# Performance work log

Hardware: AMD Instinct MI355X
Metric: run time of the kernel (lower is better)

Reference implementation:

```python
import jax, jax.numpy as jnp
import numpy as np

SR = 22050
HOP = 512
BINS_PER_OCTAVE = 24
N_OCTAVES = 7
N_BINS = BINS_PER_OCTAVE * N_OCTAVES  # 168
FMIN = 32.7  # center_bins with bins_per_semitone=1 leaves fmin unchanged


def _make_cqt_kernels():
    """Right-aligned (causal) complex CQT kernels, 24 bins/octave, 7 octaves.

    This is the explicit math the stateful SlidingCqt24 C++ routine computes
    incrementally: for each bin k with center freq f_k = fmin * 2^(k/24),
    a Hann-windowed complex exponential of length N_k = ceil(Q*sr/f_k),
    Q = 1/(2^(1/24)-1). Bins are ordered ascending in frequency, matching the
    per-octave np.flip layout of the original forward.
    """
    Q = 1.0 / (2.0 ** (1.0 / BINS_PER_OCTAVE) - 1.0)
    freqs = FMIN * 2.0 ** (np.arange(N_BINS) / BINS_PER_OCTAVE)
    lens = np.ceil(Q * SR / freqs).astype(np.int64)
    n_max = int(lens.max())  # 23014
    kr = np.zeros((N_BINS, n_max), dtype=np.float32)
    ki = np.zeros((N_BINS, n_max), dtype=np.float32)
    for k in range(N_BINS):  # small fixed loop over 168 bins (setup only)
        n = int(lens[k])
        t = np.arange(n)
        win = np.hanning(n)
        c = win * np.exp(2j * np.pi * freqs[k] * t / SR) / n
        kr[k, n_max - n:] = c.real.astype(np.float32)
        ki[k, n_max - n:] = c.imag.astype(np.float32)
    return kr, ki


def setup_inputs() -> dict:
    key = jax.random.key(0)
    audio = jax.random.normal(key, (4, 1, 352768), dtype=jnp.float32)
    kr, ki = _make_cqt_kernels()
    return {
        "audio_waveforms": audio,
        "kern_real": jnp.asarray(kr),
        "kern_imag": jnp.asarray(ki),
    }


def reference(audio_waveforms, kern_real, kern_imag):
    # audio: [B, C, S]; kernels: [K, Nmax]
    n_max = kern_real.shape[1]
    B, C, S = audio_waveforms.shape
    n_blocks = S // HOP  # 689
    # Causal sliding window: block i analyzes the n_max samples ending at
    # sample (i+1)*HOP (left zero-pad for early blocks), matching the
    # block-streaming behavior of the sliding CQT.
    pad = n_max - HOP
    x = jnp.pad(audio_waveforms, ((0, 0), (0, 0), (pad, 0)))
    # Strided frame gather: [n_blocks, Nmax] index table.
    idx = jnp.arange(n_blocks)[:, None] * HOP + jnp.arange(n_max)[None, :]
    frames = x[..., idx]  # [B, C, T, Nmax]
    re = jnp.einsum("bctn,kn->bctk", frames, kern_real)
    im = jnp.einsum("bctn,kn->bctk", frames, kern_imag)
    mag = jnp.sqrt(re * re + im * im)  # [B, C, n_blocks, n_bins]
    return mag
```

## Files before the change

### kernel.cpp

```cpp
#include <hip/hip_runtime.h>
#include <math.h>


namespace {
constexpr int kSR    = 22050;
constexpr int kHop   = 512;
constexpr int kBins  = 168;
constexpr int kT     = 689;
constexpr int kB     = 4;
constexpr int kS     = 352768;
constexpr float kKScale    = 4096.0f;
constexpr float kKScaleInv = 1.0f / 4096.0f;
constexpr int kG16 = 11;
constexpr int kFBB = 44;
constexpr int kAcc = kB * kT * kBins * 2;
constexpr int kTPadB   = 768;
constexpr int kBinPadB = 176;
constexpr int kAccB    = kB * kTPadB * kBinPadB * 2;
}

typedef _Float16 half8 __attribute__((ext_vector_type(8)));
typedef _Float16 half2v __attribute__((ext_vector_type(2)));
typedef float floatx4 __attribute__((ext_vector_type(4)));

struct Jobs {
  int k0[48];
  int lo[48];
  int hi[48];
  int n;
};

struct JobsC {
  int lo16[kG16];
  int cb16[kG16];
  int mlo[3];
  int sm[24];
  int slo[24];
  int shi[24];
  int sbeg[3];
  int scnt[3];
  int ns;
  int totch;
};

__device__ inline void atomAddF(float* p, float v) {
  __hip_atomic_fetch_add(p, v, __ATOMIC_RELAXED, __HIP_MEMORY_SCOPE_AGENT);
}

typedef __attribute__((address_space(3))) unsigned int lds_uint;
typedef __attribute__((address_space(1))) const unsigned int glb_uint;
__device__ __forceinline__ void dma16(const void* g, void* l) {
  __builtin_amdgcn_global_load_lds((glb_uint*)g, (lds_uint*)l, 16, 0, 0);
}

__global__ __launch_bounds__(256) void prep_fused(
    const float* __restrict__ x, const float* __restrict__ kr,
    const float* __restrict__ ki, _Float16* __restrict__ xp,
    _Float16* __restrict__ bp, float* __restrict__ accb,
    const int pad, const int xps, const int nmax,
    const int nbx, const int nbp, const JobsC jt) {
  int bid = blockIdx.x;
  const int tid = threadIdx.x;

  if (bid < nbx) {
    const int octx = xps >> 3;
    const int gid = bid * 256 + tid;
    if (gid >= kB * octx) return;
    const int b = gid / octx;
    const int i = (gid - b * octx) * 8;
    const float* xb = x + (size_t)b * kS - pad;
    half8 h;
    #pragma unroll
    for (int j = 0; j < 8; ++j) {
      const int e = i + j;
      h[j] = (e >= pad && e < pad + kS) ? (_Float16)xb[e] : (_Float16)0.f;
    }
    *(half8*)&xp[(size_t)b * xps + i] = h;
    return;
  }
  bid -= nbx;

  if (bid < nbp) {
    const int chunkid = bid * 4 + (tid >> 6);
    const int lane = tid & 63;
    if (chunkid >= jt.totch) return;
    int g = 0;
    #pragma unroll
    for (int j = 1; j < kG16; ++j)
      if (chunkid >= jt.cb16[j]) g = j;
    const int c = chunkid - jt.cb16[g];
    const int mm = lane & 15;
    const int q  = lane >> 4;
    const int bin  = g * 16 + mm;
    const int col0 = jt.lo16[g] + c * 32 + q * 8;
    const bool binok = (bin < kBins);
    const float* rowr = kr + (size_t)bin * nmax;
    const float* rowi = ki + (size_t)bin * nmax;
    half8 hre, him;
    #pragma unroll
    for (int j = 0; j < 8; ++j) {
      const int col = col0 + j;
      const bool ok = binok && (col < nmax);
      hre[j] = ok ? (_Float16)(rowr[col] * kKScale) : (_Float16)0.f;
      him[j] = ok ? (_Float16)(rowi[col] * kKScale) : (_Float16)0.f;
    }
    _Float16* dst = bp + (size_t)chunkid * 1024 + lane * 8;
    *(half8*)dst = hre;
    *(half8*)(dst + 512) = him;
    return;
  }
  bid -= nbp;

  const int idx = (bid * 256 + tid) * 4;
  if (idx < kAcc)
    *(floatx4*)&accb[idx] = (floatx4){0.f, 0.f, 0.f, 0.f};
}

template <bool PARTIAL>
__global__ __launch_bounds__(256) void cqt_mfma_t(
    const _Float16* __restrict__ bp, const _Float16* __restrict__ xp,
    float* __restrict__ accb, _Float16* __restrict__ part,
    const int xps, const JobsC jt) {
  __shared__ _Float16 lds[2][12288];

  const int sx = blockIdx.y;
  const int fb = blockIdx.x >> 2;
  const int b  = blockIdx.x & 3;
  const int tid  = threadIdx.x;
  const int wave = tid >> 6;
  const int lane = tid & 63;
  const int mm = lane & 15;
  const int q  = lane >> 4;
  const int mac = jt.sm[sx];
  const int g16 = mac * 4 + wave;
  const bool gvalid = (g16 < kG16);
  const int mlo = jt.mlo[mac];
  const int gs = gvalid ? ((jt.lo16[g16] - mlo) >> 5) : 0x7fffffff;
  const int slo = jt.slo[sx];
  const int shi = jt.shi[sx];
  const int fbase = fb * 64;

  const _Float16* xb = xp + (size_t)b * xps;
  int aoff0, aoff1;
  {
    const int r0 = wave * 2;
    int row0 = fbase + (r0 & 3) * 16 + mm;
    if (row0 > kT - 1) row0 = kT - 1;
    aoff0 = row0 * kHop + (r0 >> 2) * 32 + q * 8;
    const int r1 = r0 + 1;
    int row1 = fbase + (r1 & 3) * 16 + mm;
    if (row1 > kT - 1) row1 = kT - 1;
    aoff1 = row1 * kHop + (r1 >> 2) * 32 + q * 8;
  }
  const _Float16* bgrp =
      gvalid ? (bp + (size_t)(jt.cb16[g16] - gs) * 1024 + lane * 8) : bp;

  floatx4 accr[4], acci[4];
  #pragma unroll
  for (int tl = 0; tl < 4; ++tl) {
    accr[tl] = (floatx4){0.f, 0.f, 0.f, 0.f};
    acci[tl] = (floatx4){0.f, 0.f, 0.f, 0.f};
  }

  auto stageDMA = [&](int c, int buf) {
    _Float16* L = lds[buf];
    const _Float16* xc = xb + mlo + c * 32;
    dma16(xc + aoff0, L + (wave * 2) * 512);
    dma16(xc + aoff1, L + (wave * 2 + 1) * 512);
    if (gvalid && c >= gs) {
      const _Float16* bs = bgrp + (size_t)c * 1024;
      #pragma unroll
      for (int cc = 0; cc < 2; ++cc)
        #pragma unroll
        for (int ri = 0; ri < 2; ++ri)
          dma16(bs + cc * 1024 + ri * 512,
                L + 4096 + (wave * 4 + cc * 2 + ri) * 512);
    }
  };

  auto compute = [&](int c, int buf) {
    if (!gvalid || c < gs) return;
    const _Float16* L = lds[buf];
    #pragma unroll
    for (int cc = 0; cc < 2; ++cc) {
      const half8 Bre = *(const half8*)(L + 4096 + (wave * 4 + cc * 2) * 512 + lane * 8);
      const half8 Bim = *(const half8*)(L + 4096 + (wave * 4 + cc * 2 + 1) * 512 + lane * 8);
      #pragma unroll
      for (int tl = 0; tl < 4; ++tl) {
        const half8 A = *(const half8*)(L + (cc * 4 + tl) * 512 + lane * 8);
        accr[tl] = __builtin_amdgcn_mfma_f32_16x16x32_f16(A, Bre, accr[tl], 0, 0, 0);
        acci[tl] = __builtin_amdgcn_mfma_f32_16x16x32_f16(A, Bim, acci[tl], 0, 0, 0);
      }
    }
  };

  stageDMA(slo, 0);
  int buf = 0;
  #pragma unroll 1
  for (int c = slo; c < shi; c += 2) {
    __syncthreads();
    if (c + 2 < shi) stageDMA(c + 2, buf ^ 1);
    compute(c, buf);
    buf ^= 1;
  }

  if (PARTIAL) {
    _Float16* pw = part +
        (((size_t)sx * kFBB + blockIdx.x) * 4 + wave) * 2048 + lane * 32;
    #pragma unroll
    for (int tl = 0; tl < 4; ++tl) {
      half8 p;
      #pragma unroll
      for (int r = 0; r < 4; ++r) {
        p[r * 2]     = (_Float16)accr[tl][r];
        p[r * 2 + 1] = (_Float16)acci[tl][r];
      }
      *(half8*)(pw + tl * 8) = p;
    }
  } else {
    const int bin = g16 * 16 + mm;
    if (bin < kBins) {
      #pragma unroll
      for (int tl = 0; tl < 4; ++tl) {
        const int tb = fbase + tl * 16 + q * 4;
        #pragma unroll
        for (int r = 0; r < 4; ++r) {
          const int t = tb + r;
          if (t < kT) {
            const size_t o = (((size_t)b * kT + t) * kBins + bin) * 2;
            atomAddF(&accb[o],     accr[tl][r] * kKScaleInv);
            atomAddF(&accb[o + 1], acci[tl][r] * kKScaleInv);
          }
        }
      }
    }
  }
}

__global__ __launch_bounds__(256) void cqt_mag_part(
    const _Float16* __restrict__ part, float* __restrict__ out,
    const JobsC jt) {
  const int fbb = blockIdx.x;
  const int fb = fbb >> 2;
  const int b  = fbb & 3;
  const int wave = threadIdx.x >> 6;
  const int lane = threadIdx.x & 63;
  const int g16 = blockIdx.y * 4 + wave;
  if (g16 >= kG16) return;
  const int mac = g16 >> 2;
  const int w   = g16 & 3;
  const int mm = lane & 15;
  const int q  = lane >> 4;

  float a[32];
  #pragma unroll
  for (int i = 0; i < 32; ++i) a[i] = 0.f;
  const int s0 = jt.sbeg[mac];
  const int s1 = s0 + jt.scnt[mac];
  #pragma unroll 1
  for (int s = s0; s < s1; ++s) {
    const _Float16* p = part +
        (((size_t)s * kFBB + fbb) * 4 + w) * 2048 + lane * 32;
    #pragma unroll
    for (int tl = 0; tl < 4; ++tl) {
      const half8 v = *(const half8*)(p + tl * 8);
      #pragma unroll
      for (int j = 0; j < 8; ++j) a[tl * 8 + j] += (float)v[j];
    }
  }
  const int k = g16 * 16 + mm;
  if (k >= kBins) return;
  #pragma unroll
  for (int tl = 0; tl < 4; ++tl) {
    #pragma unroll
    for (int r = 0; r < 4; ++r) {
      const int t = fb * 64 + tl * 16 + q * 4 + r;
      if (t < kT) {
        const float re = a[tl * 8 + r * 2];
        const float im = a[tl * 8 + r * 2 + 1];
        out[((size_t)b * kT + t) * kBins + k] =
            sqrtf(re * re + im * im) * kKScaleInv;
      }
    }
  }
}

__global__ __launch_bounds__(256) void cqt_mag4(
    const float* __restrict__ accb, float* __restrict__ out) {
  const int gid = (blockIdx.x * 256 + threadIdx.x) * 4;
  if (gid >= kB * kT * kBins) return;
  const floatx4 v0 = *(const floatx4*)&accb[gid * 2];
  const floatx4 v1 = *(const floatx4*)&accb[gid * 2 + 4];
  floatx4 o;
  o[0] = sqrtf(v0[0] * v0[0] + v0[1] * v0[1]);
  o[1] = sqrtf(v0[2] * v0[2] + v0[3] * v0[3]);
  o[2] = sqrtf(v1[0] * v1[0] + v1[1] * v1[1]);
  o[3] = sqrtf(v1[2] * v1[2] + v1[3] * v1[3]);
  *(floatx4*)&out[gid] = o;
}

__global__ __launch_bounds__(256) void cqt_mag_final(
    const float* __restrict__ accb, float* __restrict__ out,
    const int tp, const int kp) {
  int gid = blockIdx.x * 256 + threadIdx.x;
  if (gid >= kB * kT * kBins) return;
  const int k = gid % kBins;
  const int r = gid / kBins;
  const int t = r % kT;
  const int b = r / kT;
  const float2 v = ((const float2*)accb)[((size_t)b * tp + t) * kp + k];
  out[gid] = sqrtf(v.x * v.x + v.y * v.y);
}

__global__ __launch_bounds__(256) void prep_x_kernel(
    const float* __restrict__ x, _Float16* __restrict__ xp,
    const int pad, const int xps) {
  const int halfx = xps >> 1;
  int gid = blockIdx.x * 256 + threadIdx.x;
  if (gid >= kB * halfx) return;
  const int b = gid / halfx;
  const int i = (gid - b * halfx) * 2;
  float v0 = 0.f, v1 = 0.f;
  if (i     >= pad && i     < pad + kS) v0 = x[(size_t)b * kS + (i - pad)];
  if (i + 1 >= pad && i + 1 < pad + kS) v1 = x[(size_t)b * kS + (i + 1 - pad)];
  half2v h; h.x = (_Float16)v0; h.y = (_Float16)v1;
  *(half2v*)&xp[(size_t)b * xps + i] = h;
}

__global__ __launch_bounds__(256) void cqt_mfma_kernel(
    const float* __restrict__ kr, const float* __restrict__ ki,
    const _Float16* __restrict__ xp, float* __restrict__ accb,
    const int nmax, const int xps, const Jobs jt) {
  __shared__ _Float16 Bs[2][16][264];
  const int jb = blockIdx.x;
  const int k0   = jt.k0[jb];
  const int n_lo = jt.lo[jb];
  const int n_hi = jt.hi[jb];
  const int b  = blockIdx.z;
  const int fb = blockIdx.y;
  const int tid  = threadIdx.x;
  const int lane = tid & 63;
  const int wave = tid >> 6;
  const int m = lane & 15;
  const int q = lane >> 4;
  const int sbin = tid >> 4;
  const int scol = tid & 15;
  const int gbin = k0 + sbin;
  const bool binok = (gbin < kBins);
  const float* rowr = kr + (size_t)gbin * nmax;
  const float* rowi = ki + (size_t)gbin * nmax;
  const int fbase = fb * 256 + wave * 64;
  const _Float16* ax =
      xp + (size_t)b * xps + (size_t)(fbase + m) * kHop + q * 8;
  floatx4 accr[4], acci[4];
  #pragma unroll
  for (int tl = 0; tl < 4; ++tl) {
    accr[tl] = (floatx4){0.f, 0.f, 0.f, 0.f};
    acci[tl] = (floatx4){0.f, 0.f, 0.f, 0.f};
  }
  for (int n0r = n_lo; n0r < n_hi; n0r += 256) {
    __syncthreads();
    #pragma unroll
    for (int c = 0; c < 16; ++c) {
      const int col = n0r + scol + c * 16;
      const bool ok = binok && (col < nmax);
      const float vr = ok ? rowr[col] : 0.f;
      const float vi = ok ? rowi[col] : 0.f;
      Bs[0][sbin][scol + c * 16] = (_Float16)(vr * kKScale);
      Bs[1][sbin][scol + c * 16] = (_Float16)(vi * kKScale);
    }
    __syncthreads();
    const _Float16* axr = ax + n0r;
    #pragma unroll
    for (int c = 0; c < 8; ++c) {
      const int ko = c * 32 + q * 8;
      const half8 br = *(const half8*)&Bs[0][m][ko];
      const half8 bi = *(const half8*)&Bs[1][m][ko];
      #pragma unroll
      for (int tl = 0; tl < 4; ++tl) {
        const half8 a = *(const half8*)(axr + tl * 16 * kHop + c * 32);
        accr[tl] = __builtin_amdgcn_mfma_f32_16x16x32_f16(a, br, accr[tl], 0, 0, 0);
        acci[tl] = __builtin_amdgcn_mfma_f32_16x16x32_f16(a, bi, acci[tl], 0, 0, 0);
      }
    }
  }
  #pragma unroll
  for (int tl = 0; tl < 4; ++tl) {
    #pragma unroll
    for (int rr = 0; rr < 4; ++rr) {
      const int t = fbase + tl * 16 + q * 4 + rr;
      const size_t o = (((size_t)b * kTPadB + t) * kBinPadB + (k0 + m)) * 2;
      atomAddF(&accb[o],     accr[tl][rr] * kKScaleInv);
      atomAddF(&accb[o + 1], acci[tl][rr] * kKScaleInv);
    }
  }
}

namespace fb32 {
constexpr int TT = 8;
constexpr int KG = 4;
constexpr int kTTiles  = (kT + TT - 1) / TT;
constexpr int kKGroups = kBins / KG;
constexpr int kWaves   = kB * kTTiles * kKGroups;
}

__global__ __launch_bounds__(256) void cqt_mag_kernel(
    const float* __restrict__ x,
    const float* __restrict__ kr,
    const float* __restrict__ ki,
    float* __restrict__ out,
    const int nmax, const int pad) {
  using namespace fb32;
  const int wave = (blockIdx.x << 2) + (threadIdx.x >> 6);
  const int lane = threadIdx.x & 63;
  if (wave >= kWaves) return;
  const int kg    = wave / (kB * kTTiles);
  const int rem   = wave - kg * (kB * kTTiles);
  const int b     = rem / kTTiles;
  const int ttile = rem - b * kTTiles;
  const int k0 = kg * KG;
  const int t0 = ttile * TT;
  const double Q  = 1.0 / (exp2(1.0 / 24.0) - 1.0);
  const double f0 = 32.7 * exp2((double)k0 / 24.0);
  int N = (int)ceil(Q * (double)kSR / f0) + 8;
  int full_start = nmax - N;
  if (full_start < 0) full_start = 0;
  int tbase[TT], lo[TT], t_last;
  { int t = t0 + TT - 1; if (t > kT - 1) t = kT - 1; t_last = t; }
  #pragma unroll
  for (int tt = 0; tt < TT; ++tt) {
    int t = t0 + tt; if (t > kT - 1) t = kT - 1;
    tbase[tt] = b * kS + t * kHop - pad;
    lo[tt]    = pad - t * kHop;
  }
  int head_start = pad - t_last * kHop;
  if (head_start < full_start) head_start = full_start;
  int safe = pad - t0 * kHop;
  if (safe < head_start) safe = head_start;
  int body_start = nmax - ((nmax - safe) & ~63);
  float accr[TT][KG], acci[TT][KG];
  #pragma unroll
  for (int tt = 0; tt < TT; ++tt)
    #pragma unroll
    for (int kk = 0; kk < KG; ++kk) { accr[tt][kk] = 0.f; acci[tt][kk] = 0.f; }
  for (int n = body_start - 64; n > head_start - 64; n -= 64) {
    const int nn = n + lane;
    const bool kok = (nn >= 0);
    float krv[KG], kiv[KG];
    #pragma unroll
    for (int kk = 0; kk < KG; ++kk) {
      krv[kk] = kok ? kr[(k0 + kk) * nmax + nn] : 0.f;
      kiv[kk] = kok ? ki[(k0 + kk) * nmax + nn] : 0.f;
    }
    float a[TT];
    #pragma unroll
    for (int tt = 0; tt < TT; ++tt)
      a[tt] = (nn >= lo[tt]) ? x[tbase[tt] + nn] : 0.f;
    #pragma unroll
    for (int tt = 0; tt < TT; ++tt)
      #pragma unroll
      for (int kk = 0; kk < KG; ++kk) {
        accr[tt][kk] = fmaf(a[tt], krv[kk], accr[tt][kk]);
        acci[tt][kk] = fmaf(a[tt], kiv[kk], acci[tt][kk]);
      }
  }
  for (int n = body_start; n < nmax; n += 64) {
    const int nn = n + lane;
    float krv[KG], kiv[KG];
    #pragma unroll
    for (int kk = 0; kk < KG; ++kk) {
      krv[kk] = kr[(k0 + kk) * nmax + nn];
      kiv[kk] = ki[(k0 + kk) * nmax + nn];
    }
    float a[TT];
    #pragma unroll
    for (int tt = 0; tt < TT; ++tt)
      a[tt] = x[tbase[tt] + nn];
    #pragma unroll
    for (int tt = 0; tt < TT; ++tt)
      #pragma unroll
      for (int kk = 0; kk < KG; ++kk) {
        accr[tt][kk] = fmaf(a[tt], krv[kk], accr[tt][kk]);
        acci[tt][kk] = fmaf(a[tt], kiv[kk], acci[tt][kk]);
      }
  }
  #pragma unroll
  for (int tt = 0; tt < TT; ++tt) {
    #pragma unroll
    for (int kk = 0; kk < KG; ++kk) {
      float r = accr[tt][kk];
      float i = acci[tt][kk];
      #pragma unroll
      for (int s = 32; s > 0; s >>= 1) {
        r += __shfl_xor(r, s, 64);
        i += __shfl_xor(i, s, 64);
      }
      if (lane == 0) {
        const int t = t0 + tt;
        if (t < kT)
          out[(b * kT + t) * kBins + (k0 + kk)] = sqrtf(r * r + i * i);
      }
    }
  }
}

extern "C" void kernel_launch(void* const* d_in, const int* in_sizes, int n_in,
                              void* d_out, int out_size, void* d_ws, size_t ws_size,
                              hipStream_t stream) {
  const float* x  = (const float*)d_in[0];
  const float* kr = (const float*)d_in[1];
  const float* ki = (const float*)d_in[2];
  float* out = (float*)d_out;

  const int nmax = in_sizes[1] / kBins;
  const int pad  = nmax - kHop;

  const int kcap = ((nmax + 255) / 256) * 256;
  const double Q = 1.0 / (exp2(1.0 / 24.0) - 1.0);

  JobsC jc;
  int tot = 0;
  for (int g = 0; g < kG16; ++g) {
    const double f0 = 32.7 * exp2((double)(16 * g) / 24.0);
    const int N = (int)ceil(Q * (double)kSR / f0) + 8;
    int lo = nmax - N;
    if (lo < 0) lo = 0;
    lo &= ~255;
    jc.lo16[g] = lo;
    jc.cb16[g] = tot;
    tot += (kcap - lo) / 32;
  }
  jc.totch = tot;
  int ns = 0;
  for (int m = 0; m < 3; ++m) {
    jc.mlo[m] = jc.lo16[4 * m];
    jc.sbeg[m] = ns;
    const int C = (kcap - jc.mlo[m]) / 32;
    const int nsl = (C + 95) / 96;
    const int len = ((C + nsl - 1) / nsl + 1) & ~1;
    for (int s = 0; s < nsl && ns < 24; ++s) {
      const int lo = s * len;
      if (lo >= C) break;
      int hi = lo + len;
      if (hi > C) hi = C;
      jc.sm[ns] = m; jc.slo[ns] = lo; jc.shi[ns] = hi;
      ++ns;
    }
    jc.scnt[m] = ns - jc.sbeg[m];
  }
  jc.ns = ns;

  const int xpsA = (kT - 1) * kHop + kcap + 256;
  const size_t xpA_bytes = (size_t)kB * xpsA * sizeof(_Float16);
  const size_t bpA_bytes = (size_t)tot * 2048;

  const size_t partP_off   = (xpA_bytes + 511) & ~(size_t)511;
  const size_t partP_bytes = (size_t)ns * kFBB * 4 * 2048 * sizeof(_Float16);
  const size_t bpP_off     = (partP_off + partP_bytes + 511) & ~(size_t)511;
  const size_t ws_P = bpP_off + bpA_bytes;

  const size_t accA_off  = (xpA_bytes + 511) & ~(size_t)511;
  const size_t accA_bytes = (size_t)kAcc * sizeof(float);
  const size_t bpA_off   = (accA_off + accA_bytes + 511) & ~(size_t)511;
  const size_t ws_A = bpA_off + bpA_bytes;

  const int xpsB = (kTPadB - 1) * kHop + kcap + 256;
  const size_t xpB_bytes = (size_t)kB * xpsB * sizeof(_Float16);
  const size_t accB_off  = (xpB_bytes + 511) & ~(size_t)511;
  const size_t accB_bytes = (size_t)kAccB * sizeof(float);
  const size_t ws_B = accB_off + accB_bytes;

  const int nbx = (kB * (xpsA / 8) + 255) / 256;
  const int nbp = (tot + 3) / 4;

  if (ws_size >= ws_P) {
    _Float16* xp   = (_Float16*)d_ws;
    _Float16* part = (_Float16*)((char*)d_ws + partP_off);
    _Float16* bp   = (_Float16*)((char*)d_ws + bpP_off);

    prep_fused<<<nbx + nbp, 256, 0, stream>>>(
        x, kr, ki, xp, bp, (float*)part , pad, xpsA, nmax,
        nbx, nbp, jc);
    {
      dim3 grid(kFBB, ns);
      cqt_mfma_t<true><<<grid, 256, 0, stream>>>(
          bp, xp, nullptr, part, xpsA, jc);
    }
    {
      dim3 grid(kFBB, 3);
      cqt_mag_part<<<grid, 256, 0, stream>>>(part, out, jc);
    }
    return;
  }

  if (ws_size >= ws_A) {
    _Float16* xp = (_Float16*)d_ws;
    float* accb  = (float*)((char*)d_ws + accA_off);
    _Float16* bp = (_Float16*)((char*)d_ws + bpA_off);

    const int nba = (kAcc / 4 + 255) / 256;
    prep_fused<<<nbx + nbp + nba, 256, 0, stream>>>(
        x, kr, ki, xp, bp, accb, pad, xpsA, nmax, nbx, nbp, jc);
    {
      dim3 grid(kFBB, ns);
      cqt_mfma_t<false><<<grid, 256, 0, stream>>>(
          bp, xp, accb, nullptr, xpsA, jc);
    }
    {
      const int total = kB * kT * kBins;
      cqt_mag4<<<(total / 4 + 255) / 256, 256, 0, stream>>>(accb, out);
    }
    return;
  }

  if (ws_size >= ws_B) {
    _Float16* xp = (_Float16*)d_ws;
    float* accb  = (float*)((char*)d_ws + accB_off);
    Jobs jt;
    int nj = 0;
    for (int g = 0; g < 11; ++g) {
      const int gk0 = 16 * g;
      const double f0 = 32.7 * exp2((double)gk0 / 24.0);
      const int N = (int)ceil(Q * (double)kSR / f0) + 8;
      int lo = nmax - N;
      if (lo < 0) lo = 0;
      lo = (lo / 2048) * 2048;
      for (int s = lo; s < kcap && nj < 48; s += 2048) {
        jt.k0[nj] = gk0;
        jt.lo[nj] = s;
        jt.hi[nj] = (s + 2048 < kcap) ? s + 2048 : kcap;
        ++nj;
      }
    }
    jt.n = nj;
    hipMemsetAsync(accb, 0, accB_bytes, stream);
    {
      const int total = kB * (xpsB / 2);
      prep_x_kernel<<<(total + 255) / 256, 256, 0, stream>>>(x, xp, pad, xpsB);
    }
    {
      dim3 grid(nj, kTPadB / 256, kB);
      cqt_mfma_kernel<<<grid, 256, 0, stream>>>(kr, ki, xp, accb, nmax, xpsB, jt);
    }
    {
      const int total = kB * kT * kBins;
      cqt_mag_final<<<(total + 255) / 256, 256, 0, stream>>>(
          accb, out, kTPadB, kBinPadB);
    }
    return;
  }

  {
    const int blocks = fb32::kWaves / 4;
    cqt_mag_kernel<<<blocks, 256, 0, stream>>>(x, kr, ki, out, nmax, pad);
  }
}
```

Baseline: 119.8 us.

## Triple-buffer LDS DMA pipeline with uniform loads and XCD-aware block remap

Moves the MFMA CQT kernel from double to triple LDS buffering, so two stages are in flight, using an explicit vmcnt wait and raw barrier in place of __syncthreads. The B-kernel DMA is made unconditional, clamping the chunk index, so every wave issues the same number of loads and the fixed vmcnt count holds. Workgroup indices are also remapped so neighbouring blocks land on the same XCD, for better L2 reuse. This costs 50% more shared memory, which may lower occupancy, plus some redundant B loads for waves that have not started or are invalid.

After: 125.8 us. 5.0% more time.

```diff
diff --git a/kernel.cpp b/kernel.cpp
--- a/kernel.cpp
+++ b/kernel.cpp
@@ -121,11 +121,19 @@
     const _Float16* __restrict__ bp, const _Float16* __restrict__ xp,
     float* __restrict__ accb, _Float16* __restrict__ part,
     const int xps, const JobsC jt) {
-  __shared__ _Float16 lds[2][12288];
-
-  const int sx = blockIdx.y;
-  const int fb = blockIdx.x >> 2;
-  const int b  = blockIdx.x & 3;
+  __shared__ _Float16 lds[3][12288];
+
+  const int nwg = kFBB * gridDim.y;
+  int lin = blockIdx.y * kFBB + blockIdx.x;
+  {
+    const int q = nwg >> 3, r = nwg & 7;
+    const int xcd = lin & 7, idx = lin >> 3;
+    lin = (xcd < r ? xcd * (q + 1) : r * (q + 1) + (xcd - r) * q) + idx;
+  }
+  const int sx  = lin / kFBB;
+  const int fbb = lin - sx * kFBB;
+  const int fb = fbb >> 2;
+  const int b  = fbb & 3;
   const int tid  = threadIdx.x;
   const int wave = tid >> 6;
   const int lane = tid & 63;
@@ -135,7 +143,7 @@
   const int g16 = mac * 4 + wave;
   const bool gvalid = (g16 < kG16);
   const int mlo = jt.mlo[mac];
-  const int gs = gvalid ? ((jt.lo16[g16] - mlo) >> 5) : 0x7fffffff;
+  const int gs = gvalid ? ((jt.lo16[g16] - mlo) >> 5) : 0;
   const int slo = jt.slo[sx];
   const int shi = jt.shi[sx];
   const int fbase = fb * 64;
@@ -153,7 +161,8 @@
     aoff1 = row1 * kHop + (r1 >> 2) * 32 + q * 8;
   }
   const _Float16* bgrp =
-      gvalid ? (bp + (size_t)(jt.cb16[g16] - gs) * 1024 + lane * 8) : bp;
+      gvalid ? (bp + (size_t)(jt.cb16[g16] - gs) * 1024 + lane * 8)
+             : (bp + lane * 8);
 
   floatx4 accr[4], acci[4];
   #pragma unroll
@@ -167,15 +176,14 @@
     const _Float16* xc = xb + mlo + c * 32;
     dma16(xc + aoff0, L + (wave * 2) * 512);
     dma16(xc + aoff1, L + (wave * 2 + 1) * 512);
-    if (gvalid && c >= gs) {
-      const _Float16* bs = bgrp + (size_t)c * 1024;
-      #pragma unroll
-      for (int cc = 0; cc < 2; ++cc)
-        #pragma unroll
-        for (int ri = 0; ri < 2; ++ri)
-          dma16(bs + cc * 1024 + ri * 512,
-                L + 4096 + (wave * 4 + cc * 2 + ri) * 512);
-    }
+    const int cb = gvalid ? (c > gs ? c : gs) : 0;
+    const _Float16* bs = bgrp + (size_t)cb * 1024;
+    #pragma unroll
+    for (int cc = 0; cc < 2; ++cc)
+      #pragma unroll
+      for (int ri = 0; ri < 2; ++ri)
+        dma16(bs + cc * 1024 + ri * 512,
+              L + 4096 + (wave * 4 + cc * 2 + ri) * 512);
   };
 
   auto compute = [&](int c, int buf) {
@@ -194,19 +202,23 @@
     }
   };
 
+  const int cN = shi - 2;
   stageDMA(slo, 0);
-  int buf = 0;
+  stageDMA(slo + 2 <= cN ? slo + 2 : cN, 1);
+  int j = 0;
   #pragma unroll 1
-  for (int c = slo; c < shi; c += 2) {
-    __syncthreads();
-    if (c + 2 < shi) stageDMA(c + 2, buf ^ 1);
-    compute(c, buf);
-    buf ^= 1;
+  for (int c = slo; c < shi; c += 2, ++j) {
+    asm volatile("s_waitcnt vmcnt(6)" ::: "memory");
+    __builtin_amdgcn_s_barrier();
+    __builtin_amdgcn_sched_barrier(0);
+    int cn = c + 4; if (cn > cN) cn = cN;
+    stageDMA(cn, (j + 2) % 3);
+    compute(c, j % 3);
   }
 
   if (PARTIAL) {
     _Float16* pw = part +
-        (((size_t)sx * kFBB + blockIdx.x) * 4 + wave) * 2048 + lane * 32;
+        (((size_t)sx * kFBB + fbb) * 4 + wave) * 2048 + lane * 32;
     #pragma unroll
     for (int tl = 0; tl < 4; ++tl) {
       half8 p;
@@ -219,7 +231,7 @@
     }
   } else {
     const int bin = g16 * 16 + mm;
-    if (bin < kBins) {
+    if (gvalid && bin < kBins) {
       #pragma unroll
       for (int tl = 0; tl < 4; ++tl) {
         const int tb = fbase + tl * 16 + q * 4;
```

## Load B fragments directly to registers and remap workgroups across XCDs

Applied to the files above, without the earlier changes.

Per-wave B (kernel) fragments are now read from global memory straight into registers inside compute, instead of being DMA-staged through LDS. This shrinks the LDS footprint from 48KB to 16KB per block, which can raise occupancy. Workgroup indices are also remapped so consecutive logical blocks land on the same XCD, improving L2 locality on the MI355X chiplet layout. The trade-off is that global load latency for B is no longer hidden by the double buffer and sits directly on the MFMA path. A gvalid guard is added to the atomic write-back.

Result: slower. 125.7 us (+5.0%).

```diff
diff --git a/kernel.cpp b/kernel.cpp
--- a/kernel.cpp
+++ b/kernel.cpp
@@ -121,11 +121,19 @@
     const _Float16* __restrict__ bp, const _Float16* __restrict__ xp,
     float* __restrict__ accb, _Float16* __restrict__ part,
     const int xps, const JobsC jt) {
-  __shared__ _Float16 lds[2][12288];
-
-  const int sx = blockIdx.y;
-  const int fb = blockIdx.x >> 2;
-  const int b  = blockIdx.x & 3;
+  __shared__ _Float16 lds[2][4096];
+
+  const int nwg = kFBB * gridDim.y;
+  int lin = blockIdx.y * kFBB + blockIdx.x;
+  {
+    const int q = nwg >> 3, r = nwg & 7;
+    const int xcd = lin & 7, idx = lin >> 3;
+    lin = (xcd < r ? xcd * (q + 1) : r * (q + 1) + (xcd - r) * q) + idx;
+  }
+  const int sx  = lin / kFBB;
+  const int fbb = lin - sx * kFBB;
+  const int fb = fbb >> 2;
+  const int b  = fbb & 3;
   const int tid  = threadIdx.x;
   const int wave = tid >> 6;
   const int lane = tid & 63;
@@ -167,30 +175,24 @@
     const _Float16* xc = xb + mlo + c * 32;
     dma16(xc + aoff0, L + (wave * 2) * 512);
     dma16(xc + aoff1, L + (wave * 2 + 1) * 512);
-    if (gvalid && c >= gs) {
-      const _Float16* bs = bgrp + (size_t)c * 1024;
-      #pragma unroll
-      for (int cc = 0; cc < 2; ++cc)
-        #pragma unroll
-        for (int ri = 0; ri < 2; ++ri)
-          dma16(bs + cc * 1024 + ri * 512,
-                L + 4096 + (wave * 4 + cc * 2 + ri) * 512);
-    }
   };
 
   auto compute = [&](int c, int buf) {
     if (!gvalid || c < gs) return;
+    const _Float16* bs = bgrp + (size_t)c * 1024;
+    const half8 Bre0 = *(const half8*)bs;
+    const half8 Bim0 = *(const half8*)(bs + 512);
+    const half8 Bre1 = *(const half8*)(bs + 1024);
+    const half8 Bim1 = *(const half8*)(bs + 1536);
     const _Float16* L = lds[buf];
     #pragma unroll
-    for (int cc = 0; cc < 2; ++cc) {
-      const half8 Bre = *(const half8*)(L + 4096 + (wave * 4 + cc * 2) * 512 + lane * 8);
-      const half8 Bim = *(const half8*)(L + 4096 + (wave * 4 + cc * 2 + 1) * 512 + lane * 8);
-      #pragma unroll
-      for (int tl = 0; tl < 4; ++tl) {
-        const half8 A = *(const half8*)(L + (cc * 4 + tl) * 512 + lane * 8);
-        accr[tl] = __builtin_amdgcn_mfma_f32_16x16x32_f16(A, Bre, accr[tl], 0, 0, 0);
-        acci[tl] = __builtin_amdgcn_mfma_f32_16x16x32_f16(A, Bim, acci[tl], 0, 0, 0);
-      }
+    for (int tl = 0; tl < 4; ++tl) {
+      const half8 A0 = *(const half8*)(L + tl * 512 + lane * 8);
+      accr[tl] = __builtin_amdgcn_mfma_f32_16x16x32_f16(A0, Bre0, accr[tl], 0, 0, 0);
+      acci[tl] = __builtin_amdgcn_mfma_f32_16x16x32_f16(A0, Bim0, acci[tl], 0, 0, 0);
+      const half8 A1 = *(const half8*)(L + (4 + tl) * 512 + lane * 8);
+      accr[tl] = __builtin_amdgcn_mfma_f32_16x16x32_f16(A1, Bre1, accr[tl], 0, 0, 0);
+      acci[tl] = __builtin_amdgcn_mfma_f32_16x16x32_f16(A1, Bim1, acci[tl], 0, 0, 0);
     }
   };
 
@@ -206,7 +208,7 @@
 
   if (PARTIAL) {
     _Float16* pw = part +
-        (((size_t)sx * kFBB + blockIdx.x) * 4 + wave) * 2048 + lane * 32;
+        (((size_t)sx * kFBB + fbb) * 4 + wave) * 2048 + lane * 32;
     #pragma unroll
     for (int tl = 0; tl < 4; ++tl) {
       half8 p;
@@ -219,7 +221,7 @@
     }
   } else {
     const int bin = g16 * 16 + mm;
-    if (bin < kBins) {
+    if (gvalid && bin < kBins) {
       #pragma unroll
       for (int tl = 0; tl < 4; ++tl) {
         const int tb = fbase + tl * 16 + q * 4;
```

## Load CQT kernel fragments directly to registers and shrink LDS staging

Applied to the files above, without the earlier changes.

Kernel (B-operand) fragments are now loaded straight from global memory into registers with double-buffered register sets, instead of being DMA'd through LDS. Only the audio frames are still staged in LDS, which cuts LDS to 16 KB per block; launch bounds now request 4 blocks per CU. The host also splits the chunk range into twice as many slices to expose more parallelism. The cost is more register pressure, direct global loads on the critical path, and more partial results to reduce.

New measurement: 123.4 us. +3.0%, slower.

```diff
diff --git a/kernel.cpp b/kernel.cpp
--- a/kernel.cpp
+++ b/kernel.cpp
@@ -116,12 +116,32 @@
     *(floatx4*)&accb[idx] = (floatx4){0.f, 0.f, 0.f, 0.f};
 }
 
+#define BLD(S, c)                                                      \
+  { const _Float16* bs_ = bgrp + (size_t)(c) * 1024;                   \
+    S##0 = *(const half8*)(bs_);                                       \
+    S##1 = *(const half8*)(bs_ + 512);                                 \
+    S##2 = *(const half8*)(bs_ + 1024);                                \
+    S##3 = *(const half8*)(bs_ + 1536); }
+
+#define MMC(S, bufid)                                                  \
+  { const _Float16* L_ = lds[bufid];                                   \
+    _Pragma("unroll")                                                  \
+    for (int cc = 0; cc < 2; ++cc) {                                   \
+      const half8 Bre_ = (cc == 0) ? S##0 : S##2;                      \
+      const half8 Bim_ = (cc == 0) ? S##1 : S##3;                      \
+      _Pragma("unroll")                                                \
+      for (int tl = 0; tl < 4; ++tl) {                                 \
+        const half8 A_ = *(const half8*)(L_ + (cc * 4 + tl) * 512 + lane * 8); \
+        accr[tl] = __builtin_amdgcn_mfma_f32_16x16x32_f16(A_, Bre_, accr[tl], 0, 0, 0); \
+        acci[tl] = __builtin_amdgcn_mfma_f32_16x16x32_f16(A_, Bim_, acci[tl], 0, 0, 0); \
+      } } }
+
 template <bool PARTIAL>
-__global__ __launch_bounds__(256) void cqt_mfma_t(
+__global__ __launch_bounds__(256, 4) void cqt_mfma_t(
     const _Float16* __restrict__ bp, const _Float16* __restrict__ xp,
     float* __restrict__ accb, _Float16* __restrict__ part,
     const int xps, const JobsC jt) {
-  __shared__ _Float16 lds[2][12288];
+  __shared__ _Float16 lds[2][4096];
 
   const int sx = blockIdx.y;
   const int fb = blockIdx.x >> 2;
@@ -135,10 +155,11 @@
   const int g16 = mac * 4 + wave;
   const bool gvalid = (g16 < kG16);
   const int mlo = jt.mlo[mac];
-  const int gs = gvalid ? ((jt.lo16[g16] - mlo) >> 5) : 0x7fffffff;
+  const int gs = gvalid ? ((jt.lo16[g16] - mlo) >> 5) : 0;
   const int slo = jt.slo[sx];
   const int shi = jt.shi[sx];
   const int fbase = fb * 64;
+  int cw0 = slo; if (gvalid && gs > cw0) cw0 = gs;
 
   const _Float16* xb = xp + (size_t)b * xps;
   int aoff0, aoff1;
@@ -153,7 +174,8 @@
     aoff1 = row1 * kHop + (r1 >> 2) * 32 + q * 8;
   }
   const _Float16* bgrp =
-      gvalid ? (bp + (size_t)(jt.cb16[g16] - gs) * 1024 + lane * 8) : bp;
+      gvalid ? (bp + (size_t)(jt.cb16[g16] - gs) * 1024 + lane * 8)
+             : (bp + lane * 8);
 
   floatx4 accr[4], acci[4];
   #pragma unroll
@@ -162,45 +184,32 @@
     acci[tl] = (floatx4){0.f, 0.f, 0.f, 0.f};
   }
 
-  auto stageDMA = [&](int c, int buf) {
+  auto stageA = [&](int c, int buf) {
     _Float16* L = lds[buf];
     const _Float16* xc = xb + mlo + c * 32;
     dma16(xc + aoff0, L + (wave * 2) * 512);
     dma16(xc + aoff1, L + (wave * 2 + 1) * 512);
-    if (gvalid && c >= gs) {
-      const _Float16* bs = bgrp + (size_t)c * 1024;
-      #pragma unroll
-      for (int cc = 0; cc < 2; ++cc)
-        #pragma unroll
-        for (int ri = 0; ri < 2; ++ri)
-          dma16(bs + cc * 1024 + ri * 512,
-                L + 4096 + (wave * 4 + cc * 2 + ri) * 512);
-    }
   };
 
-  auto compute = [&](int c, int buf) {
-    if (!gvalid || c < gs) return;
-    const _Float16* L = lds[buf];
-    #pragma unroll
-    for (int cc = 0; cc < 2; ++cc) {
-      const half8 Bre = *(const half8*)(L + 4096 + (wave * 4 + cc * 2) * 512 + lane * 8);
-      const half8 Bim = *(const half8*)(L + 4096 + (wave * 4 + cc * 2 + 1) * 512 + lane * 8);
-      #pragma unroll
-      for (int tl = 0; tl < 4; ++tl) {
-        const half8 A = *(const half8*)(L + (cc * 4 + tl) * 512 + lane * 8);
-        accr[tl] = __builtin_amdgcn_mfma_f32_16x16x32_f16(A, Bre, accr[tl], 0, 0, 0);
-        acci[tl] = __builtin_amdgcn_mfma_f32_16x16x32_f16(A, Bim, acci[tl], 0, 0, 0);
-      }
-    }
-  };
-
-  stageDMA(slo, 0);
+  half8 U0{}, U1{}, U2{}, U3{}, V0{}, V1{}, V2{}, V3{};
+
+  stageA(slo, 0);
+  if (gvalid && cw0 == slo) BLD(U, slo);
   int buf = 0;
+  int c = slo;
   #pragma unroll 1
-  for (int c = slo; c < shi; c += 2) {
+  for (; c + 2 < shi; c += 4) {
     __syncthreads();
-    if (c + 2 < shi) stageDMA(c + 2, buf ^ 1);
-    compute(c, buf);
+    stageA(c + 2, buf ^ 1);
+    if (gvalid && c + 2 >= cw0) BLD(V, c + 2);
+    __builtin_amdgcn_sched_barrier(0);
+    if (gvalid && c >= cw0) MMC(U, buf);
+    buf ^= 1;
+    __syncthreads();
+    if (c + 4 < shi) stageA(c + 4, buf ^ 1);
+    if (gvalid && c + 4 < shi && c + 4 >= cw0) BLD(U, c + 4);
+    __builtin_amdgcn_sched_barrier(0);
+    if (gvalid && c + 2 >= cw0) MMC(V, buf);
     buf ^= 1;
   }
 
@@ -219,7 +228,7 @@
     }
   } else {
     const int bin = g16 * 16 + mm;
-    if (bin < kBins) {
+    if (gvalid && bin < kBins) {
       #pragma unroll
       for (int tl = 0; tl < 4; ++tl) {
         const int tb = fbase + tl * 16 + q * 4;
@@ -236,6 +245,8 @@
     }
   }
 }
+#undef BLD
+#undef MMC
 
 __global__ __launch_bounds__(256) void cqt_mag_part(
     const _Float16* __restrict__ part, float* __restrict__ out,
@@ -536,7 +547,7 @@
     jc.mlo[m] = jc.lo16[4 * m];
     jc.sbeg[m] = ns;
     const int C = (kcap - jc.mlo[m]) / 32;
-    const int nsl = (C + 95) / 96;
+    const int nsl = (C + 47) / 48;
     const int len = ((C + nsl - 1) / nsl + 1) & ~1;
     for (int s = 0; s < nsl && ns < 24; ++s) {
       const int lo = s * len;
```
